# Kernel optimization log

Hardware: AMD Instinct MI355X
Metric: run time of the kernel (lower is better)

Reference implementation:

```python
import jax, jax.numpy as jnp
import numpy as np

H = 1024          # hidden_size
NH = 16           # num_attention_heads
HD = H // NH      # head_size
EPS = 1e-5


def setup_inputs() -> dict:
    key = jax.random.key(0)
    ks = jax.random.split(key, 5)
    # xavier_uniform bound for Linear(in, out): sqrt(6/(in+out))
    b_qkv = float(np.sqrt(6.0 / (H + 3 * H)))
    b_out = float(np.sqrt(6.0 / (H + H)))
    return {
        "hidden_states": jax.random.normal(ks[0], (2, 2048, H), dtype=jnp.float32),
        "ln_gamma": jnp.ones((H,), jnp.float32),
        "ln_beta": jnp.zeros((H,), jnp.float32),
        "W_qkv": jax.random.uniform(ks[1], (3 * H, H), jnp.float32, -b_qkv, b_qkv),
        "b_qkv": jnp.zeros((3 * H,), jnp.float32),
        "W_out": jax.random.uniform(ks[2], (H, H), jnp.float32, -b_out, b_out),
        "b_out": jnp.zeros((H,), jnp.float32),
    }


def _attn_block(x, ln_gamma, ln_beta, W_qkv, b_qkv, W_out, b_out):
    B, S, _ = x.shape
    # Pre-LN
    mu = jnp.mean(x, axis=-1, keepdims=True)
    var = jnp.mean(jnp.square(x - mu), axis=-1, keepdims=True)
    xn = (x - mu) / jnp.sqrt(var + EPS) * ln_gamma + ln_beta
    # fused QKV projection: [B,S,3H]
    qkv = jnp.einsum("bsh,oh->bso", xn, W_qkv) + b_qkv
    qkv = qkv.reshape(B, S, 3, NH, HD).transpose(2, 0, 3, 1, 4)  # [3,B,NH,S,HD]
    q, k, v = qkv[0], qkv[1], qkv[2]
    scores = jnp.einsum("bhqd,bhkd->bhqk", q, k) / jnp.sqrt(jnp.asarray(HD, x.dtype))
    probs = jax.nn.softmax(scores, axis=-1)
    ctx = jnp.einsum("bhqk,bhkd->bhqd", probs, v)
    ctx = ctx.transpose(0, 2, 1, 3).reshape(B, S, H)
    out = jnp.einsum("bsh,oh->bso", ctx, W_out) + b_out  # dropout: eval mode = identity
    return x + out


def reference(hidden_states, ln_gamma, ln_beta, W_qkv, b_qkv, W_out, b_out):
    return _attn_block(hidden_states, ln_gamma, ln_beta, W_qkv, b_qkv, W_out, b_out)
```

## Files before the change

### kernel.cpp

```cpp
#include <hip/hip_runtime.h>
#include <stdint.h>

typedef unsigned short u16;
typedef __attribute__((ext_vector_type(8))) short bf16x8;
typedef __attribute__((ext_vector_type(4))) float f32x4;
typedef __attribute__((ext_vector_type(4))) unsigned int u32x4;
typedef __attribute__((ext_vector_type(2))) unsigned int u32x2;
typedef __attribute__((ext_vector_type(4))) unsigned short u16x4;

#define QSCALE 0.18033688011112042f

typedef __attribute__((address_space(1))) const void gvoid;
typedef __attribute__((address_space(3))) void svoid;

__device__ __forceinline__ void cp16(const u16* g, u16* l) {
    __builtin_amdgcn_global_load_lds((gvoid*)g, (svoid*)l, 16, 0, 0);
}

__device__ __forceinline__ u16 f2bf(float f) {
    uint32_t u = __float_as_uint(f);
    u += 0x7fff + ((u >> 16) & 1);
    return (u16)(u >> 16);
}

__device__ __forceinline__ uint32_t pack_bf2(float lo, float hi) {
    uint32_t a = __float_as_uint(lo) + 0x8000u;
    uint32_t b = __float_as_uint(hi) + 0x8000u;
    return __builtin_amdgcn_perm(b, a, 0x07060302);
}

__global__ __launch_bounds__(256) void k_pre(const float* __restrict__ X,
                                             const float* __restrict__ gam,
                                             const float* __restrict__ bet,
                                             u16* __restrict__ XN,
                                             const float* __restrict__ Wqkv, u16* __restrict__ Wq,
                                             const float* __restrict__ Wout, u16* __restrict__ Wo) {
    __shared__ float red[8];
    const int bid = blockIdx.x;
    if (bid < 4096) {
        int t = bid;
        const float4* xp = (const float4*)(X + (size_t)t * 1024);
        float4 x = xp[threadIdx.x];
        float s  = x.x + x.y + x.z + x.w;
        float s2 = x.x*x.x + x.y*x.y + x.z*x.z + x.w*x.w;
        #pragma unroll
        for (int off = 1; off < 64; off <<= 1) {
            s  += __shfl_xor(s,  off, 64);
            s2 += __shfl_xor(s2, off, 64);
        }
        int lane = threadIdx.x & 63, w = threadIdx.x >> 6;
        if (lane == 0) { red[w] = s; red[w + 4] = s2; }
        __syncthreads();
        s  = red[0] + red[1] + red[2] + red[3];
        s2 = red[4] + red[5] + red[6] + red[7];
        float mu  = s * (1.0f / 1024.0f);
        float var = s2 * (1.0f / 1024.0f) - mu * mu;
        float rin = rsqrtf(var + 1e-5f);
        float4 g = ((const float4*)gam)[threadIdx.x];
        float4 b = ((const float4*)bet)[threadIdx.x];
        u16x4 o;
        o.x = f2bf((x.x - mu) * rin * g.x + b.x);
        o.y = f2bf((x.y - mu) * rin * g.y + b.y);
        o.z = f2bf((x.z - mu) * rin * g.z + b.z);
        o.w = f2bf((x.w - mu) * rin * g.w + b.w);
        *(u16x4*)(XN + (size_t)t * 1024 + threadIdx.x * 4) = o;
    } else {
        int i = (bid - 4096) * 256 + threadIdx.x;
        const float* src; u16* dst;
        if (i < 786432) { src = Wqkv; dst = Wq; }
        else            { i -= 786432; src = Wout; dst = Wo; }
        float4 v = ((const float4*)src)[i];
        u16x4 o;
        o.x = f2bf(v.x); o.y = f2bf(v.y); o.z = f2bf(v.z); o.w = f2bf(v.w);
        ((u16x4*)dst)[i] = o;
    }
}

__device__ __forceinline__ void gemm_bt_tile(const u16* __restrict__ A, const u16* __restrict__ Bm,
                                             int m0, int n0, u16* As, u16* Bs, f32x4 acc[4][4]) {
    const int tid = threadIdx.x;
    const int lane = tid & 63;
    const int wv = tid >> 6;
    const int qi = lane & 15, g = lane >> 4, swz = qi & 7;
    const int wr = (wv >> 1) * 64, wc = (wv & 1) * 64;
    #pragma unroll
    for (int mi = 0; mi < 4; mi++)
        #pragma unroll
        for (int ni = 0; ni < 4; ni++) acc[mi][ni] = (f32x4){0.f, 0.f, 0.f, 0.f};

    const int row_in = tid >> 3;
    const int cs = (tid & 7) ^ (row_in & 7);
    for (int k0 = 0; k0 < 1024; k0 += 64) {
        __syncthreads();
        #pragma unroll
        for (int i = 0; i < 4; i++) {
            int row = i * 32 + row_in;
            cp16(A  + (size_t)(m0 + row) * 1024 + k0 + cs * 8, As + (i * 256 + wv * 64) * 8);
            cp16(Bm + (size_t)(n0 + row) * 1024 + k0 + cs * 8, Bs + (i * 256 + wv * 64) * 8);
        }
        __syncthreads();
        #pragma unroll
        for (int ks = 0; ks < 2; ks++) {
            bf16x8 af[4], bf[4];
            #pragma unroll
            for (int mi = 0; mi < 4; mi++)
                af[mi] = *(const bf16x8*)(As + (wr + mi * 16 + qi) * 64 + ((ks * 4 + g) ^ swz) * 8);
            #pragma unroll
            for (int ni = 0; ni < 4; ni++)
                bf[ni] = *(const bf16x8*)(Bs + (wc + ni * 16 + qi) * 64 + ((ks * 4 + g) ^ swz) * 8);
            #pragma unroll
            for (int mi = 0; mi < 4; mi++)
                #pragma unroll
                for (int ni = 0; ni < 4; ni++)
                    acc[mi][ni] = __builtin_amdgcn_mfma_f32_16x16x32_bf16(af[mi], bf[ni], acc[mi][ni], 0, 0, 0);
        }
    }
}


#define CFENCE asm volatile("" ::: "memory")
#define BARX() do { CFENCE; __builtin_amdgcn_s_barrier(); CFENCE; } while (0)
#define LGKM0() asm volatile("s_waitcnt lgkmcnt(0)" ::: "memory")

__global__ __launch_bounds__(512, 2) void k_qkv(const u16* __restrict__ XN, const u16* __restrict__ Wq,
                                                const float* __restrict__ bqkv,
                                                u16* __restrict__ Q, u16* __restrict__ K,
                                                u16* __restrict__ Vt) {
    __shared__ __align__(16) u16 SMEM[65536];
    const int tid = threadIdx.x;
    const int lane = tid & 63, w = tid >> 6;
    const int qi = lane & 15, g = lane >> 4, swz = qi & 7;
    const int wr = (w >> 2) * 128, wc = (w & 3) * 64;

    const int id = blockIdx.x;
    const int sw = (id & 7) * 24 + (id >> 3);
    const int n0 = (sw % 12) * 256;
    const int m0 = (sw / 12) * 256;

    const int laneRow = lane >> 3, laneCg = lane & 7;
    const int cs = laneCg ^ laneRow;
    const int aw = (w & 3) * 8 + (w >> 2) * 128;
    const u16* gA = XN + (size_t)(m0 + aw + laneRow) * 1024 + cs * 8;
    const u16* gB = Wq + (size_t)(n0 + w * 8 + laneRow) * 1024 + cs * 8;

#define SM_A(s) (SMEM + (s) * 32768)
#define SM_B(s) (SMEM + (s) * 32768 + 16384)
#define STAGE_A(tau, q, s) cp16(gA + (size_t)(q) * 32 * 1024 + (tau) * 64, SM_A(s) + ((q) * 32 + aw) * 64)
#define STAGE_B(tau, part, s)                                                                       \
    do { cp16(gB + (size_t)(part) * 128 * 1024 + (tau) * 64, SM_B(s) + ((part) * 128 + w * 8) * 64); \
         cp16(gB + (size_t)((part) * 128 + 64) * 1024 + (tau) * 64,                                  \
              SM_B(s) + ((part) * 128 + 64 + w * 8) * 64); } while (0)

    f32x4 acc[8][4];
    #pragma unroll
    for (int mi = 0; mi < 8; mi++)
        #pragma unroll
        for (int ni = 0; ni < 4; ni++) acc[mi][ni] = (f32x4){0.f, 0.f, 0.f, 0.f};
    bf16x8 bf[4][2];

    STAGE_B(0, 0, 0); STAGE_B(0, 1, 0);
    STAGE_A(0, 0, 0); STAGE_A(0, 1, 0); STAGE_A(0, 2, 0); STAGE_A(0, 3, 0);
    STAGE_B(1, 0, 1); STAGE_B(1, 1, 1);
    STAGE_A(1, 0, 1); STAGE_A(1, 1, 1);
    asm volatile("s_waitcnt vmcnt(6)" ::: "memory");
    BARX();

#define PHASE_A(q)                                                                                   \
    bf16x8 af[2][2];                                                                                 \
    _Pragma("unroll") for (int m2 = 0; m2 < 2; m2++)                                                 \
    _Pragma("unroll") for (int ks = 0; ks < 2; ks++)                                                 \
        af[m2][ks] = *(const bf16x8*)(as_ + (wr + ((q) * 2 + m2) * 16 + qi) * 64 + (((ks * 4 + g) ^ swz)) * 8);

#define DO_MFMA(q)                                                                                   \
    __builtin_amdgcn_s_setprio(1);                                                                   \
    _Pragma("unroll") for (int m2 = 0; m2 < 2; m2++)                                                 \
    _Pragma("unroll") for (int ni = 0; ni < 4; ni++) {                                               \
        acc[(q) * 2 + m2][ni] = __builtin_amdgcn_mfma_f32_16x16x32_bf16(af[m2][0], bf[ni][0], acc[(q) * 2 + m2][ni], 0, 0, 0); \
        acc[(q) * 2 + m2][ni] = __builtin_amdgcn_mfma_f32_16x16x32_bf16(af[m2][1], bf[ni][1], acc[(q) * 2 + m2][ni], 0, 0, 0); \
    }                                                                                                \
    __builtin_amdgcn_s_setprio(0);

    for (int t = 0; t < 16; t++) {
        const int s = t & 1;
        const u16* as_ = SM_A(s);
        const u16* bs_ = SM_B(s);
        {
            PHASE_A(0)
            #pragma unroll
            for (int ni = 0; ni < 4; ni++)
                #pragma unroll
                for (int ks = 0; ks < 2; ks++)
                    bf[ni][ks] = *(const bf16x8*)(bs_ + (wc + ni * 16 + qi) * 64 + ((ks * 4 + g) ^ swz) * 8);
            if (t < 15) { STAGE_A(t + 1, 2, s ^ 1); STAGE_A(t + 1, 3, s ^ 1); }
            BARX(); LGKM0();
            DO_MFMA(0)
            BARX();
        }
        {
            PHASE_A(1)
            if (t < 14) STAGE_B(t + 2, 0, s);
            BARX(); LGKM0();
            DO_MFMA(1)
            BARX();
        }
        {
            PHASE_A(2)
            if (t < 14) STAGE_B(t + 2, 1, s);
            BARX(); LGKM0();
            DO_MFMA(2)
            BARX();
        }
        {
            PHASE_A(3)
            if (t < 14) { STAGE_A(t + 2, 0, s); STAGE_A(t + 2, 1, s); }
            BARX(); LGKM0();
            DO_MFMA(3)
            if (t < 14) { asm volatile("s_waitcnt vmcnt(6)" ::: "memory"); }
            else        { asm volatile("s_waitcnt vmcnt(0)" ::: "memory"); }
            BARX();
        }
    }

    if (n0 < 2048) {
        const int which = n0 >> 10;
        u16* base = which ? K : Q;
        const float scale = which ? 1.0f : QSCALE;
        #pragma unroll
        for (int mi = 0; mi < 8; mi++)
            #pragma unroll
            for (int ni = 0; ni < 4; ni++)
                #pragma unroll
                for (int i = 0; i < 4; i++) {
                    int m = m0 + wr + mi * 16 + (g * 4 + i);
                    int n = n0 + wc + ni * 16 + qi;
                    float v = (acc[mi][ni][i] + bqkv[n]) * scale;
                    int b = m >> 11, ss = m & 2047;
                    int hh = (n >> 6) & 15, d = n & 63;
                    base[((size_t)(b * 16 + hh) * 2048 + ss) * 64 + d] = f2bf(v);
                }
    } else {
        u16* Tw = SMEM + w * 4352;
        const int head = (n0 + wc - 2048) >> 6;
        const int b = m0 >> 11;
        #pragma unroll
        for (int h = 0; h < 2; h++) {
            #pragma unroll
            for (int mi2 = 0; mi2 < 4; mi2++)
                #pragma unroll
                for (int ni = 0; ni < 4; ni++) {
                    int mi = h * 4 + mi2;
                    int n = n0 + wc + ni * 16 + qi;
                    float bq = bqkv[n];
                    u16x4 pk;
                    pk.x = f2bf(acc[mi][ni][0] + bq);
                    pk.y = f2bf(acc[mi][ni][1] + bq);
                    pk.z = f2bf(acc[mi][ni][2] + bq);
                    pk.w = f2bf(acc[mi][ni][3] + bq);
                    *(u16x4*)(Tw + (ni * 16 + qi) * 68 + mi2 * 16 + g * 4) = pk;
                }
            int s0 = (m0 + wr + h * 64) & 2047;
            u16* vrow = Vt + (size_t)(b * 16 + head) * 64 * 2048 + s0 + qi * 4;
            #pragma unroll
            for (int dd = 0; dd < 16; dd++) {
                int d = dd * 4 + g;
                u16x4 val = *(const u16x4*)(Tw + d * 68 + qi * 4);
                *(u16x4*)(vrow + (size_t)d * 2048) = val;
            }
        }
    }
#undef SM_A
#undef SM_B
#undef STAGE_A
#undef STAGE_B
#undef PHASE_A
#undef DO_MFMA
}

__global__ __launch_bounds__(512) void k_attn(const u16* __restrict__ Q, const u16* __restrict__ K,
                                              const u16* __restrict__ Vt, u16* __restrict__ CTX) {
    __shared__ __align__(16) u16 Ks[2][64 * 64];
    __shared__ __align__(16) u16 Vs[2][64 * 64];
    __shared__ __align__(16) u16 Ps[8][16 * 64];
    const int id = blockIdx.x;
    const int bh = (id & 7) * 4 + ((id >> 3) & 3);
    const int q0 = (id >> 5) * 128;
    const int lane = threadIdx.x & 63, w = threadIdx.x >> 6;
    const int g = lane >> 4, qi = lane & 15, swz = qi & 7;
    const u16* Qp = Q  + (size_t)bh * (2048 * 64);
    const u16* Kp = K  + (size_t)bh * (2048 * 64);
    const u16* Vp = Vt + (size_t)bh * (64 * 2048);
    u16* Pw = Ps[w];

    const int r0 = w * 8 + (lane >> 3);
    const int cs = (lane & 7) ^ (r0 & 7);
    const u16* kg0 = Kp + (size_t)r0 * 64 + cs * 8;
    const u16* vg0 = Vp + (size_t)r0 * 2048 + cs * 8;

    bf16x8 bq[2];
    {
        const u16* qb = Qp + (size_t)(q0 + w * 16 + qi) * 64 + g * 8;
        bq[0] = *(const bf16x8*)(qb);
        bq[1] = *(const bf16x8*)(qb + 32);
    }
    float lsumA = 0.f, lsumB = 0.f;
    f32x4 od[4];
    #pragma unroll
    for (int nt = 0; nt < 4; nt++) od[nt] = (f32x4){0.f, 0.f, 0.f, 0.f};

    cp16(kg0, Ks[0] + w * 512);
    cp16(vg0, Vs[0] + w * 512);

    #define ATTN_STEP(KT, CKS, CVS, PKS, PVS)                                                    \
    {                                                                                            \
        const int kt_ = (KT);                                                                    \
        __syncthreads();                                                                         \
        if (kt_ < 31) {                                                                          \
            cp16(kg0 + 4096, (PKS) + w * 512);                 \
            cp16(vg0 + 64,   (PVS) + w * 512);            \
        }                                                                                        \
        const u16* ksp = (CKS);                                                                  \
        const u16* vsp = (CVS);                                                                  \
        f32x4 sv[4];                                                                             \
        _Pragma("unroll")                                                                        \
        for (int nt = 0; nt < 4; nt++) sv[nt] = (f32x4){0.f, 0.f, 0.f, 0.f};                     \
        _Pragma("unroll")                                                                        \
        for (int ks = 0; ks < 2; ks++)                                                           \
            _Pragma("unroll")                                                                    \
            for (int nt = 0; nt < 4; nt++) {                                                     \
                bf16x8 ak = *(const bf16x8*)(ksp + (nt * 16 + qi) * 64 + ((ks * 4 + g) ^ swz) * 8); \
                sv[nt] = __builtin_amdgcn_mfma_f32_16x16x32_bf16(ak, bq[ks], sv[nt], 0, 0, 0);   \
            }                                                                                    \
        _Pragma("unroll")                                                                        \
        for (int nt = 0; nt < 2; nt++) {                                                         \
            float e0 = __builtin_amdgcn_exp2f(sv[nt][0]);                                        \
            float e1 = __builtin_amdgcn_exp2f(sv[nt][1]);                                        \
            float e2 = __builtin_amdgcn_exp2f(sv[nt][2]);                                        \
            float e3 = __builtin_amdgcn_exp2f(sv[nt][3]);                                        \
            lsumA += e0 + e1; lsumB += e2 + e3;                                                  \
            u32x2 pk = {pack_bf2(e0, e1), pack_bf2(e2, e3)};                                     \
            *(u32x2*)(Pw + qi * 64 + ((2 * nt + (g >> 1)) ^ swz) * 8 + (g & 1) * 4) = pk;        \
        }                                                                                        \
        {                                                                                        \
            bf16x8 bp = *(const bf16x8*)(Pw + qi * 64 + ((0 * 4 + g) ^ swz) * 8);                \
            _Pragma("unroll")                                                                    \
            for (int nt = 0; nt < 4; nt++) {                                                     \
                bf16x8 av = *(const bf16x8*)(vsp + (nt * 16 + qi) * 64 + ((0 * 4 + g) ^ swz) * 8); \
                od[nt] = __builtin_amdgcn_mfma_f32_16x16x32_bf16(av, bp, od[nt], 0, 0, 0);       \
            }                                                                                    \
        }                                                                                        \
        _Pragma("unroll")                                                                        \
        for (int nt = 2; nt < 4; nt++) {                                                         \
            float e0 = __builtin_amdgcn_exp2f(sv[nt][0]);                                        \
            float e1 = __builtin_amdgcn_exp2f(sv[nt][1]);                                        \
            float e2 = __builtin_amdgcn_exp2f(sv[nt][2]);                                        \
            float e3 = __builtin_amdgcn_exp2f(sv[nt][3]);                                        \
            lsumA += e0 + e1; lsumB += e2 + e3;                                                  \
            u32x2 pk = {pack_bf2(e0, e1), pack_bf2(e2, e3)};                                     \
            *(u32x2*)(Pw + qi * 64 + ((2 * nt + (g >> 1)) ^ swz) * 8 + (g & 1) * 4) = pk;        \
        }                                                                                        \
        {                                                                                        \
            bf16x8 bp = *(const bf16x8*)(Pw + qi * 64 + ((1 * 4 + g) ^ swz) * 8);                \
            _Pragma("unroll")                                                                    \
            for (int nt = 0; nt < 4; nt++) {                                                     \
                bf16x8 av = *(const bf16x8*)(vsp + (nt * 16 + qi) * 64 + ((1 * 4 + g) ^ swz) * 8); \
                od[nt] = __builtin_amdgcn_mfma_f32_16x16x32_bf16(av, bp, od[nt], 0, 0, 0);       \
            }                                                                                    \
        }                                                                                        \
        kg0 += 64 * 64; vg0 += 64;                                                               \
    }

    for (int kt = 0; kt < 32; kt += 2) {
        ATTN_STEP(kt,     Ks[0], Vs[0], Ks[1], Vs[1]);
        ATTN_STEP(kt + 1, Ks[1], Vs[1], Ks[0], Vs[0]);
    }
    #undef ATTN_STEP

    float lsum = lsumA + lsumB;
    lsum += __shfl_xor(lsum, 16, 64);
    lsum += __shfl_xor(lsum, 32, 64);
    float inv = 1.0f / lsum;
    const int b = bh >> 4, hh = bh & 15;
    size_t m = (size_t)b * 2048 + q0 + w * 16 + qi;
    u16* cp = CTX + m * 1024 + hh * 64 + g * 4;
    #pragma unroll
    for (int nt = 0; nt < 4; nt++) {
        u16x4 o;
        o.x = f2bf(od[nt][0] * inv); o.y = f2bf(od[nt][1] * inv);
        o.z = f2bf(od[nt][2] * inv); o.w = f2bf(od[nt][3] * inv);
        *(u16x4*)(cp + nt * 16) = o;
    }
}

__global__ __launch_bounds__(256) void k_out(const u16* __restrict__ CTX, const u16* __restrict__ Wo,
                                             const float* __restrict__ bout, const float* __restrict__ X,
                                             float* __restrict__ OUT) {
    __shared__ __align__(16) u16 As[128 * 64], Bs[128 * 64];
    f32x4 acc[4][4];
    const int m0 = blockIdx.y * 128, n0 = blockIdx.x * 128;
    gemm_bt_tile(CTX, Wo, m0, n0, As, Bs, acc);
    const int lane = threadIdx.x & 63, wid = threadIdx.x >> 6;
    const int wr = (wid >> 1) * 64, wc = (wid & 1) * 64;
    #pragma unroll
    for (int mi = 0; mi < 4; mi++)
        #pragma unroll
        for (int ni = 0; ni < 4; ni++)
            #pragma unroll
            for (int i = 0; i < 4; i++) {
                size_t m = m0 + wr + mi * 16 + ((lane >> 4) * 4 + i);
                int n = n0 + wc + ni * 16 + (lane & 15);
                OUT[m * 1024 + n] = acc[mi][ni][i] + bout[n] + X[m * 1024 + n];
            }
}

extern "C" void kernel_launch(void* const* d_in, const int* in_sizes, int n_in,
                              void* d_out, int out_size, void* d_ws, size_t ws_size,
                              hipStream_t stream) {
    const float* X    = (const float*)d_in[0];
    const float* gam  = (const float*)d_in[1];
    const float* bet  = (const float*)d_in[2];
    const float* Wqkv = (const float*)d_in[3];
    const float* bqkv = (const float*)d_in[4];
    const float* Wout = (const float*)d_in[5];
    const float* bout = (const float*)d_in[6];
    float* OUT = (float*)d_out;

    u16* XN  = (u16*)d_ws;
    u16* Q   = XN  + (size_t)4 * 1024 * 1024;
    u16* K   = Q   + (size_t)4 * 1024 * 1024;
    u16* Vt  = K   + (size_t)4 * 1024 * 1024;
    u16* CTX = Vt  + (size_t)4 * 1024 * 1024;
    u16* Wq  = CTX + (size_t)4 * 1024 * 1024;
    u16* Wo  = Wq  + (size_t)3 * 1024 * 1024;

    k_pre<<<8192, 256, 0, stream>>>(X, gam, bet, XN, Wqkv, Wq, Wout, Wo);
    k_qkv<<<192, 512, 0, stream>>>(XN, Wq, bqkv, Q, K, Vt);
    k_attn<<<512, 512, 0, stream>>>(Q, K, Vt, CTX);
    k_out<<<dim3(8, 32), 256, 0, stream>>>(CTX, Wo, bout, X, OUT);
}
```

Before: 190.6 us.

## Process two query sub-tiles per warp in attention to reuse K/V tiles

Each warp in the attention kernel now computes 32 query rows (two 16-row sub-tiles) instead of 16. Each block covers 256 queries and the grid is halved. K and V fragments read from LDS are shared across both sub-tiles, which halves K/V global and LDS traffic per query and amortizes synchronization. In exchange it uses more registers and a larger P buffer in shared memory, and launches fewer blocks, which may reduce occupancy and latency hiding.

```diff
diff --git a/kernel.cpp b/kernel.cpp
--- a/kernel.cpp
+++ b/kernel.cpp
@@ -280,10 +280,10 @@
                                               const u16* __restrict__ Vt, u16* __restrict__ CTX) {
     __shared__ __align__(16) u16 Ks[2][64 * 64];
     __shared__ __align__(16) u16 Vs[2][64 * 64];
-    __shared__ __align__(16) u16 Ps[8][16 * 64];
+    __shared__ __align__(16) u16 Ps[8][32 * 64];
     const int id = blockIdx.x;
     const int bh = (id & 7) * 4 + ((id >> 3) & 3);
-    const int q0 = (id >> 5) * 128;
+    const int q0 = (id >> 5) * 256;
     const int lane = threadIdx.x & 63, w = threadIdx.x >> 6;
     const int g = lane >> 4, qi = lane & 15, swz = qi & 7;
     const u16* Qp = Q  + (size_t)bh * (2048 * 64);
@@ -296,16 +296,19 @@
     const u16* kg0 = Kp + (size_t)r0 * 64 + cs * 8;
     const u16* vg0 = Vp + (size_t)r0 * 2048 + cs * 8;
 
-    bf16x8 bq[2];
-    {
-        const u16* qb = Qp + (size_t)(q0 + w * 16 + qi) * 64 + g * 8;
-        bq[0] = *(const bf16x8*)(qb);
-        bq[1] = *(const bf16x8*)(qb + 32);
-    }
-    float lsumA = 0.f, lsumB = 0.f;
-    f32x4 od[4];
-    #pragma unroll
-    for (int nt = 0; nt < 4; nt++) od[nt] = (f32x4){0.f, 0.f, 0.f, 0.f};
+    bf16x8 bq[2][2];
+    #pragma unroll
+    for (int qm = 0; qm < 2; qm++) {
+        const u16* qb = Qp + (size_t)(q0 + w * 32 + qm * 16 + qi) * 64 + g * 8;
+        bq[qm][0] = *(const bf16x8*)(qb);
+        bq[qm][1] = *(const bf16x8*)(qb + 32);
+    }
+    float lsA[2] = {0.f, 0.f}, lsB[2] = {0.f, 0.f};
+    f32x4 od[2][4];
+    #pragma unroll
+    for (int qm = 0; qm < 2; qm++)
+        #pragma unroll
+        for (int nt = 0; nt < 4; nt++) od[qm][nt] = (f32x4){0.f, 0.f, 0.f, 0.f};
 
     cp16(kg0, Ks[0] + w * 512);
     cp16(vg0, Vs[0] + w * 512);
@@ -320,50 +323,47 @@
         }                                                                                        \
         const u16* ksp = (CKS);                                                                  \
         const u16* vsp = (CVS);                                                                  \
-        f32x4 sv[4];                                                                             \
+        f32x4 sv[2][4];                                                                          \
         _Pragma("unroll")                                                                        \
-        for (int nt = 0; nt < 4; nt++) sv[nt] = (f32x4){0.f, 0.f, 0.f, 0.f};                     \
+        for (int qm = 0; qm < 2; qm++)                                                           \
+            _Pragma("unroll")                                                                    \
+            for (int nt = 0; nt < 4; nt++) sv[qm][nt] = (f32x4){0.f, 0.f, 0.f, 0.f};             \
         _Pragma("unroll")                                                                        \
-        for (int ks = 0; ks < 2; ks++)                                                           \
-            _Pragma("unroll")                                                                    \
-            for (int nt = 0; nt < 4; nt++) {                                                     \
-                bf16x8 ak = *(const bf16x8*)(ksp + (nt * 16 + qi) * 64 + ((ks * 4 + g) ^ swz) * 8); \
-                sv[nt] = __builtin_amdgcn_mfma_f32_16x16x32_bf16(ak, bq[ks], sv[nt], 0, 0, 0);   \
-            }                                                                                    \
-        _Pragma("unroll")                                                                        \
-        for (int nt = 0; nt < 2; nt++) {                                                         \
-            float e0 = __builtin_amdgcn_exp2f(sv[nt][0]);                                        \
-            float e1 = __builtin_amdgcn_exp2f(sv[nt][1]);                                        \
-            float e2 = __builtin_amdgcn_exp2f(sv[nt][2]);                                        \
-            float e3 = __builtin_amdgcn_exp2f(sv[nt][3]);                                        \
-            lsumA += e0 + e1; lsumB += e2 + e3;                                                  \
-            u32x2 pk = {pack_bf2(e0, e1), pack_bf2(e2, e3)};                                     \
-            *(u32x2*)(Pw + qi * 64 + ((2 * nt + (g >> 1)) ^ swz) * 8 + (g & 1) * 4) = pk;        \
-        }                                                                                        \
-        {                                                                                        \
-            bf16x8 bp = *(const bf16x8*)(Pw + qi * 64 + ((0 * 4 + g) ^ swz) * 8);                \
-            _Pragma("unroll")                                                                    \
-            for (int nt = 0; nt < 4; nt++) {                                                     \
-                bf16x8 av = *(const bf16x8*)(vsp + (nt * 16 + qi) * 64 + ((0 * 4 + g) ^ swz) * 8); \
-                od[nt] = __builtin_amdgcn_mfma_f32_16x16x32_bf16(av, bp, od[nt], 0, 0, 0);       \
-            }                                                                                    \
+        for (int ks = 0; ks < 2; ks++) {                                                         \
+            bf16x8 ak[4];                                                                        \
+            _Pragma("unroll")                                                                    \
+            for (int nt = 0; nt < 4; nt++)                                                       \
+                ak[nt] = *(const bf16x8*)(ksp + (nt * 16 + qi) * 64 + ((ks * 4 + g) ^ swz) * 8); \
+            _Pragma("unroll")                                                                    \
+            for (int qm = 0; qm < 2; qm++)                                                       \
+                _Pragma("unroll")                                                                \
+                for (int nt = 0; nt < 4; nt++)                                                   \
+                    sv[qm][nt] = __builtin_amdgcn_mfma_f32_16x16x32_bf16(ak[nt], bq[qm][ks], sv[qm][nt], 0, 0, 0); \
         }                                                                                        \
         _Pragma("unroll")                                                                        \
-        for (int nt = 2; nt < 4; nt++) {                                                         \
-            float e0 = __builtin_amdgcn_exp2f(sv[nt][0]);                                        \
-            float e1 = __builtin_amdgcn_exp2f(sv[nt][1]);                                        \
-            float e2 = __builtin_amdgcn_exp2f(sv[nt][2]);                                        \
-            float e3 = __builtin_amdgcn_exp2f(sv[nt][3]);                                        \
-            lsumA += e0 + e1; lsumB += e2 + e3;                                                  \
-            u32x2 pk = {pack_bf2(e0, e1), pack_bf2(e2, e3)};                                     \
-            *(u32x2*)(Pw + qi * 64 + ((2 * nt + (g >> 1)) ^ swz) * 8 + (g & 1) * 4) = pk;        \
-        }                                                                                        \
-        {                                                                                        \
-            bf16x8 bp = *(const bf16x8*)(Pw + qi * 64 + ((1 * 4 + g) ^ swz) * 8);                \
-            _Pragma("unroll")                                                                    \
-            for (int nt = 0; nt < 4; nt++) {                                                     \
-                bf16x8 av = *(const bf16x8*)(vsp + (nt * 16 + qi) * 64 + ((1 * 4 + g) ^ swz) * 8); \
-                od[nt] = __builtin_amdgcn_mfma_f32_16x16x32_bf16(av, bp, od[nt], 0, 0, 0);       \
+        for (int ks = 0; ks < 2; ks++) {                                                         \
+            _Pragma("unroll")                                                                    \
+            for (int qm = 0; qm < 2; qm++)                                                       \
+                _Pragma("unroll")                                                                \
+                for (int nt = ks * 2; nt < ks * 2 + 2; nt++) {                                   \
+                    float e0 = __builtin_amdgcn_exp2f(sv[qm][nt][0]);                            \
+                    float e1 = __builtin_amdgcn_exp2f(sv[qm][nt][1]);                            \
+                    float e2 = __builtin_amdgcn_exp2f(sv[qm][nt][2]);                            \
+                    float e3 = __builtin_amdgcn_exp2f(sv[qm][nt][3]);                            \
+                    lsA[qm] += e0 + e1; lsB[qm] += e2 + e3;                                      \
+                    u32x2 pk = {pack_bf2(e0, e1), pack_bf2(e2, e3)};                             \
+                    *(u32x2*)(Pw + qm * 1024 + qi * 64 + ((2 * nt + (g >> 1)) ^ swz) * 8 + (g & 1) * 4) = pk; \
+                }                                                                                \
+            bf16x8 av[4];                                                                        \
+            _Pragma("unroll")                                                                    \
+            for (int nt = 0; nt < 4; nt++)                                                       \
+                av[nt] = *(const bf16x8*)(vsp + (nt * 16 + qi) * 64 + ((ks * 4 + g) ^ swz) * 8); \
+            _Pragma("unroll")                                                                    \
+            for (int qm = 0; qm < 2; qm++) {                                                     \
+                bf16x8 bp = *(const bf16x8*)(Pw + qm * 1024 + qi * 64 + ((ks * 4 + g) ^ swz) * 8); \
+                _Pragma("unroll")                                                                \
+                for (int nt = 0; nt < 4; nt++)                                                   \
+                    od[qm][nt] = __builtin_amdgcn_mfma_f32_16x16x32_bf16(av[nt], bp, od[qm][nt], 0, 0, 0); \
             }                                                                                    \
         }                                                                                        \
         kg0 += 64 * 64; vg0 += 64;                                                               \
@@ -375,19 +375,22 @@
     }
     #undef ATTN_STEP
 
-    float lsum = lsumA + lsumB;
-    lsum += __shfl_xor(lsum, 16, 64);
-    lsum += __shfl_xor(lsum, 32, 64);
-    float inv = 1.0f / lsum;
     const int b = bh >> 4, hh = bh & 15;
-    size_t m = (size_t)b * 2048 + q0 + w * 16 + qi;
-    u16* cp = CTX + m * 1024 + hh * 64 + g * 4;
-    #pragma unroll
-    for (int nt = 0; nt < 4; nt++) {
-        u16x4 o;
-        o.x = f2bf(od[nt][0] * inv); o.y = f2bf(od[nt][1] * inv);
-        o.z = f2bf(od[nt][2] * inv); o.w = f2bf(od[nt][3] * inv);
-        *(u16x4*)(cp + nt * 16) = o;
+    #pragma unroll
+    for (int qm = 0; qm < 2; qm++) {
+        float lsum = lsA[qm] + lsB[qm];
+        lsum += __shfl_xor(lsum, 16, 64);
+        lsum += __shfl_xor(lsum, 32, 64);
+        float inv = 1.0f / lsum;
+        size_t m = (size_t)b * 2048 + q0 + w * 32 + qm * 16 + qi;
+        u16* cp = CTX + m * 1024 + hh * 64 + g * 4;
+        #pragma unroll
+        for (int nt = 0; nt < 4; nt++) {
+            u16x4 o;
+            o.x = f2bf(od[qm][nt][0] * inv); o.y = f2bf(od[qm][nt][1] * inv);
+            o.z = f2bf(od[qm][nt][2] * inv); o.w = f2bf(od[qm][nt][3] * inv);
+            *(u16x4*)(cp + nt * 16) = o;
+        }
     }
 }
 
@@ -434,6 +437,6 @@
 
     k_pre<<<8192, 256, 0, stream>>>(X, gam, bet, XN, Wqkv, Wq, Wout, Wo);
     k_qkv<<<192, 512, 0, stream>>>(XN, Wq, bqkv, Q, K, Vt);
-    k_attn<<<512, 512, 0, stream>>>(Q, K, Vt, CTX);
+    k_attn<<<256, 512, 0, stream>>>(Q, K, Vt, CTX);
     k_out<<<dim3(8, 32), 256, 0, stream>>>(CTX, Wo, bout, X, OUT);
 }
```

Result: slower. 198.3 us (+4.1%).

## Software-pipeline attention: overlap QK^T of tile t with PV of tile t-1

Applied to the files above, without the earlier changes.

Restructures the attention inner loop so each iteration computes the scores for the current key tile, then runs the P·V MFMAs for the previous tile, then does the exp and P store for the current tile. V gets a triple buffer and P a per-warp double buffer to support the one-step skew. s_setprio raises wave priority around the MFMA blocks. The aim is to hide exp/pack latency behind independent matrix work, at the cost of extra LDS and more register pressure.

```diff
diff --git a/kernel.cpp b/kernel.cpp
--- a/kernel.cpp
+++ b/kernel.cpp
@@ -279,8 +279,8 @@
 __global__ __launch_bounds__(512) void k_attn(const u16* __restrict__ Q, const u16* __restrict__ K,
                                               const u16* __restrict__ Vt, u16* __restrict__ CTX) {
     __shared__ __align__(16) u16 Ks[2][64 * 64];
-    __shared__ __align__(16) u16 Vs[2][64 * 64];
-    __shared__ __align__(16) u16 Ps[8][16 * 64];
+    __shared__ __align__(16) u16 Vs[3][64 * 64];
+    __shared__ __align__(16) u16 Ps[8][2][16 * 64];
     const int id = blockIdx.x;
     const int bh = (id & 7) * 4 + ((id >> 3) & 3);
     const int q0 = (id >> 5) * 128;
@@ -289,12 +289,11 @@
     const u16* Qp = Q  + (size_t)bh * (2048 * 64);
     const u16* Kp = K  + (size_t)bh * (2048 * 64);
     const u16* Vp = Vt + (size_t)bh * (64 * 2048);
-    u16* Pw = Ps[w];
 
     const int r0 = w * 8 + (lane >> 3);
     const int cs = (lane & 7) ^ (r0 & 7);
-    const u16* kg0 = Kp + (size_t)r0 * 64 + cs * 8;
-    const u16* vg0 = Vp + (size_t)r0 * 2048 + cs * 8;
+    const u16* kg = Kp + (size_t)r0 * 64 + cs * 8;
+    const u16* vg = Vp + (size_t)r0 * 2048 + cs * 8;
 
     bf16x8 bq[2];
     {
@@ -307,73 +306,75 @@
     #pragma unroll
     for (int nt = 0; nt < 4; nt++) od[nt] = (f32x4){0.f, 0.f, 0.f, 0.f};
 
-    cp16(kg0, Ks[0] + w * 512);
-    cp16(vg0, Vs[0] + w * 512);
-
-    #define ATTN_STEP(KT, CKS, CVS, PKS, PVS)                                                    \
-    {                                                                                            \
-        const int kt_ = (KT);                                                                    \
-        __syncthreads();                                                                         \
-        if (kt_ < 31) {                                                                          \
-            cp16(kg0 + 4096, (PKS) + w * 512);                 \
-            cp16(vg0 + 64,   (PVS) + w * 512);            \
-        }                                                                                        \
-        const u16* ksp = (CKS);                                                                  \
-        const u16* vsp = (CVS);                                                                  \
-        f32x4 sv[4];                                                                             \
-        _Pragma("unroll")                                                                        \
-        for (int nt = 0; nt < 4; nt++) sv[nt] = (f32x4){0.f, 0.f, 0.f, 0.f};                     \
-        _Pragma("unroll")                                                                        \
-        for (int ks = 0; ks < 2; ks++)                                                           \
-            _Pragma("unroll")                                                                    \
-            for (int nt = 0; nt < 4; nt++) {                                                     \
-                bf16x8 ak = *(const bf16x8*)(ksp + (nt * 16 + qi) * 64 + ((ks * 4 + g) ^ swz) * 8); \
-                sv[nt] = __builtin_amdgcn_mfma_f32_16x16x32_bf16(ak, bq[ks], sv[nt], 0, 0, 0);   \
-            }                                                                                    \
-        _Pragma("unroll")                                                                        \
-        for (int nt = 0; nt < 2; nt++) {                                                         \
-            float e0 = __builtin_amdgcn_exp2f(sv[nt][0]);                                        \
-            float e1 = __builtin_amdgcn_exp2f(sv[nt][1]);                                        \
-            float e2 = __builtin_amdgcn_exp2f(sv[nt][2]);                                        \
-            float e3 = __builtin_amdgcn_exp2f(sv[nt][3]);                                        \
-            lsumA += e0 + e1; lsumB += e2 + e3;                                                  \
-            u32x2 pk = {pack_bf2(e0, e1), pack_bf2(e2, e3)};                                     \
-            *(u32x2*)(Pw + qi * 64 + ((2 * nt + (g >> 1)) ^ swz) * 8 + (g & 1) * 4) = pk;        \
-        }                                                                                        \
-        {                                                                                        \
-            bf16x8 bp = *(const bf16x8*)(Pw + qi * 64 + ((0 * 4 + g) ^ swz) * 8);                \
-            _Pragma("unroll")                                                                    \
-            for (int nt = 0; nt < 4; nt++) {                                                     \
-                bf16x8 av = *(const bf16x8*)(vsp + (nt * 16 + qi) * 64 + ((0 * 4 + g) ^ swz) * 8); \
-                od[nt] = __builtin_amdgcn_mfma_f32_16x16x32_bf16(av, bp, od[nt], 0, 0, 0);       \
-            }                                                                                    \
-        }                                                                                        \
-        _Pragma("unroll")                                                                        \
-        for (int nt = 2; nt < 4; nt++) {                                                         \
-            float e0 = __builtin_amdgcn_exp2f(sv[nt][0]);                                        \
-            float e1 = __builtin_amdgcn_exp2f(sv[nt][1]);                                        \
-            float e2 = __builtin_amdgcn_exp2f(sv[nt][2]);                                        \
-            float e3 = __builtin_amdgcn_exp2f(sv[nt][3]);                                        \
-            lsumA += e0 + e1; lsumB += e2 + e3;                                                  \
-            u32x2 pk = {pack_bf2(e0, e1), pack_bf2(e2, e3)};                                     \
-            *(u32x2*)(Pw + qi * 64 + ((2 * nt + (g >> 1)) ^ swz) * 8 + (g & 1) * 4) = pk;        \
-        }                                                                                        \
-        {                                                                                        \
-            bf16x8 bp = *(const bf16x8*)(Pw + qi * 64 + ((1 * 4 + g) ^ swz) * 8);                \
-            _Pragma("unroll")                                                                    \
-            for (int nt = 0; nt < 4; nt++) {                                                     \
-                bf16x8 av = *(const bf16x8*)(vsp + (nt * 16 + qi) * 64 + ((1 * 4 + g) ^ swz) * 8); \
-                od[nt] = __builtin_amdgcn_mfma_f32_16x16x32_bf16(av, bp, od[nt], 0, 0, 0);       \
-            }                                                                                    \
-        }                                                                                        \
-        kg0 += 64 * 64; vg0 += 64;                                                               \
-    }
-
-    for (int kt = 0; kt < 32; kt += 2) {
-        ATTN_STEP(kt,     Ks[0], Vs[0], Ks[1], Vs[1]);
-        ATTN_STEP(kt + 1, Ks[1], Vs[1], Ks[0], Vs[0]);
-    }
-    #undef ATTN_STEP
+    u16 *va = Vs[2], *vb = Vs[0], *vc = Vs[1];
+
+    cp16(kg, Ks[0] + w * 512);
+    cp16(vg, vb + w * 512);
+
+    for (int t = 0; t < 32; ++t) {
+        __syncthreads();
+        if (t < 31) {
+            cp16(kg + 4096, Ks[(t + 1) & 1] + w * 512);
+            cp16(vg + 64, vc + w * 512);
+        }
+        kg += 4096; vg += 64;
+        const u16* ksp = Ks[t & 1];
+        u16* Pc = Ps[w][t & 1];
+        const u16* Pp = Ps[w][(t & 1) ^ 1];
+
+        f32x4 sv[4];
+        #pragma unroll
+        for (int nt = 0; nt < 4; nt++) sv[nt] = (f32x4){0.f, 0.f, 0.f, 0.f};
+        __builtin_amdgcn_s_setprio(1);
+        #pragma unroll
+        for (int ks = 0; ks < 2; ks++)
+            #pragma unroll
+            for (int nt = 0; nt < 4; nt++) {
+                bf16x8 ak = *(const bf16x8*)(ksp + (nt * 16 + qi) * 64 + ((ks * 4 + g) ^ swz) * 8);
+                sv[nt] = __builtin_amdgcn_mfma_f32_16x16x32_bf16(ak, bq[ks], sv[nt], 0, 0, 0);
+            }
+        __builtin_amdgcn_s_setprio(0);
+
+        if (t > 0) {
+            __builtin_amdgcn_s_setprio(1);
+            #pragma unroll
+            for (int ks = 0; ks < 2; ks++) {
+                bf16x8 bp = *(const bf16x8*)(Pp + qi * 64 + ((ks * 4 + g) ^ swz) * 8);
+                #pragma unroll
+                for (int nt = 0; nt < 4; nt++) {
+                    bf16x8 av = *(const bf16x8*)(va + (nt * 16 + qi) * 64 + ((ks * 4 + g) ^ swz) * 8);
+                    od[nt] = __builtin_amdgcn_mfma_f32_16x16x32_bf16(av, bp, od[nt], 0, 0, 0);
+                }
+            }
+            __builtin_amdgcn_s_setprio(0);
+        }
+
+        #pragma unroll
+        for (int nt = 0; nt < 4; nt++) {
+            float e0 = __builtin_amdgcn_exp2f(sv[nt][0]);
+            float e1 = __builtin_amdgcn_exp2f(sv[nt][1]);
+            float e2 = __builtin_amdgcn_exp2f(sv[nt][2]);
+            float e3 = __builtin_amdgcn_exp2f(sv[nt][3]);
+            lsumA += e0 + e1; lsumB += e2 + e3;
+            u32x2 pk = {pack_bf2(e0, e1), pack_bf2(e2, e3)};
+            *(u32x2*)(Pc + qi * 64 + ((2 * nt + (g >> 1)) ^ swz) * 8 + (g & 1) * 4) = pk;
+        }
+
+        u16* tmp = va; va = vb; vb = vc; vc = tmp;
+    }
+
+    {
+        const u16* Pp = Ps[w][1];
+        #pragma unroll
+        for (int ks = 0; ks < 2; ks++) {
+            bf16x8 bp = *(const bf16x8*)(Pp + qi * 64 + ((ks * 4 + g) ^ swz) * 8);
+            #pragma unroll
+            for (int nt = 0; nt < 4; nt++) {
+                bf16x8 av = *(const bf16x8*)(va + (nt * 16 + qi) * 64 + ((ks * 4 + g) ^ swz) * 8);
+                od[nt] = __builtin_amdgcn_mfma_f32_16x16x32_bf16(av, bp, od[nt], 0, 0, 0);
+            }
+        }
+    }
 
     float lsum = lsumA + lsumB;
     lsum += __shfl_xor(lsum, 16, 64);
```

New measurement: 187.0 us. Within noise of the previous version (-1.9%).
